# Optimization experiments

Measured on AMD Instinct MI355X. Metric: run time of the kernel, lower is better.

## Reference

```python
import math
import jax, jax.numpy as jnp
import numpy as np

B, S, D, H = 2, 4096, 512, 8
DH = D // H


def setup_inputs() -> dict:
    key = jax.random.key(0)
    ks = jax.random.split(key, 12)
    lim = 1.0 / math.sqrt(D)
    u = lambda k, shp: jax.random.uniform(k, shp, jnp.float32, -lim, lim)
    return {
        "x": jax.random.normal(ks[0], (B, S, D), jnp.float32),
        "gamma": jax.random.uniform(ks[1], (B, S, 1), jnp.float32),
        "Wq": u(ks[2], (D, D)), "bq": u(ks[3], (D,)),
        "Wk": u(ks[4], (D, D)), "bk": u(ks[5], (D,)),
        "Wv": u(ks[6], (D, D)), "bv": u(ks[7], (D,)),
        "Wo": u(ks[8], (D, D)), "bo": u(ks[9], (D,)),
    }


def reference(x, gamma, Wq, bq, Wk, bk, Wv, bv, Wo, bo):
    b, s, d = x.shape
    # projections (torch Linear: x @ W.T + b), split heads -> [B,H,S,DH]
    def proj(W, bias):
        return (x @ W.T + bias).reshape(b, s, H, DH).transpose(0, 2, 1, 3)
    q, k, v = proj(Wq, bq), proj(Wk, bk), proj(Wv, bv)

    scores = jnp.einsum("bhsd,bhtd->bhst", q, k) / math.sqrt(DH)  # [B,H,S,S]
    causal = jnp.triu(jnp.ones((s, s), bool), k=1)  # True above diagonal
    neg_inf = jnp.float32(-jnp.inf)
    scores = jnp.where(causal[None, None], neg_inf, scores)

    # hyperbolic positional bias: -log1p(gamma_i * max(i-j, 0) + 1e-8)
    pos = jnp.arange(s)
    delta = jnp.clip(pos[:, None] - pos[None, :], 0).astype(jnp.float32)  # [S,S]
    gamma_q = gamma[:, :, 0][:, :, None]  # [B,S,1]
    hyper = -jnp.log1p(gamma_q * delta + 1e-8)  # [B,S,S]
    hyper = jnp.where(causal[None], neg_inf, hyper)
    scores = scores + hyper[:, None]  # [B,H,S,S]

    attn = jax.nn.softmax(scores, axis=-1)
    out = jnp.einsum("bhst,bhtd->bhsd", attn, v)  # [B,H,S,DH]
    out = out.transpose(0, 2, 1, 3).reshape(b, s, d)
    return out @ Wo.T + bo
```

## Files before the change

kernel.cpp:

```cpp
#include <hip/hip_runtime.h>
#include <hip/hip_bf16.h>

#define Bb 2
#define Ss 4096
#define Dd 512
#define Hh 8
#define DHh 64

typedef __attribute__((ext_vector_type(8))) short short8;
typedef __attribute__((ext_vector_type(4))) float floatx4;

static __device__ __forceinline__ ushort bfbits(float f) {
  union { __hip_bfloat16 h; ushort u; } cv;
  cv.h = __float2bfloat16(f);
  return cv.u;
}

static __device__ __forceinline__ unsigned int packhi(float a, float b) {
  union { float f; unsigned int u; } ca, cb; ca.f = a; cb.f = b;
  return (ca.u >> 16) | (cb.u & 0xffff0000u);
}

__global__ void cvt_all(const float* __restrict__ x,
                        const float* __restrict__ w0, const float* __restrict__ w1,
                        const float* __restrict__ w2, const float* __restrict__ w3,
                        ushort* __restrict__ out) {
  const int XN4 = (Bb * Ss * Dd) / 4;
  const int WN4 = (Dd * Dd) / 4;
  int i = blockIdx.x * blockDim.x + threadIdx.x;
  if (i >= XN4 + 4 * WN4) return;
  const float* s; int li;
  if (i < XN4) { s = x; li = i; }
  else {
    int t = i - XN4; int j = t >> 16; li = t & (WN4 - 1);
    s = (j == 0) ? w0 : (j == 1) ? w1 : (j == 2) ? w2 : w3;
  }
  float4 f = ((const float4*)s)[li];
  ushort4 u;
  u.x = bfbits(f.x); u.y = bfbits(f.y); u.z = bfbits(f.z); u.w = bfbits(f.w);
  ((ushort4*)out)[i] = u;
}

static __device__ __forceinline__ int vperm(int s0) {
  int kb = (s0 >> 4) & 3, gq = (s0 >> 2) & 3;
  return (s0 & ~63) | ((kb >> 1) << 5) | (gq << 3) | ((kb & 1) << 2);
}

#define LDQK(buf, k0)                                                          \
  _Pragma("unroll")                                                            \
  for (int rb = 0; rb < 4; ++rb)                                               \
    af[buf][rb] = *(const short8*)(ap + (size_t)rb * 16 * 512 + (k0));         \
  _Pragma("unroll")                                                            \
  for (int cb = 0; cb < 4; ++cb)                                               \
    bf[buf][cb] = *(const short8*)(bp + (size_t)cb * 16 * 512 + (k0));

__global__ __launch_bounds__(256) void qkv_gemm(
    const ushort* __restrict__ xb,
    const ushort* __restrict__ Wq, const ushort* __restrict__ Wk, const ushort* __restrict__ Wv,
    const float* __restrict__ bq, const float* __restrict__ bk, const float* __restrict__ bv,
    ushort* __restrict__ qo, ushort* __restrict__ ko, ushort* __restrict__ vo)
{
  int mb = blockIdx.x / 12, rest = blockIdx.x % 12;
  int which = rest >> 2, nb = rest & 3;
  const ushort* Bw  = (which == 0) ? Wq : (which == 1) ? Wk : Wv;
  const float* bias = (which == 0) ? bq : (which == 1) ? bk : bv;
  int lane = threadIdx.x & 63, w = threadIdx.x >> 6;
  int wr = w & 1, wc = w >> 1;
  int g = lane >> 4, ln = lane & 15;
  int m0 = mb * 128 + wr * 64;
  int c0 = nb * 128 + wc * 64;
  const ushort* ap = xb + (size_t)(m0 + ln) * 512 + g * 8;
  const ushort* bp = Bw + (size_t)(c0 + ln) * 512 + g * 8;
  floatx4 acc[4][4] = {};
  short8 af[2][4], bf[2][4];
  LDQK(0, 0)
#pragma unroll
  for (int it = 0; it < 16; ++it) {
    int cur = it & 1;
    if (it < 15) { LDQK(cur ^ 1, (it + 1) * 32) }
#pragma unroll
    for (int rb = 0; rb < 4; ++rb)
#pragma unroll
      for (int cb = 0; cb < 4; ++cb)
        acc[rb][cb] = __builtin_amdgcn_mfma_f32_16x16x32_bf16(af[cur][rb], bf[cur][cb], acc[rb][cb], 0, 0, 0);
  }
  float scale = (which == 0) ? 0.125f : 1.0f;
#pragma unroll
  for (int rb = 0; rb < 4; ++rb)
#pragma unroll
    for (int cb = 0; cb < 4; ++cb) {
      int col = c0 + cb * 16 + ln;
      float bv_ = bias[col];
      int hh = col >> 6, dh = col & 63;
      if (which == 2) {
        int i0 = m0 + rb * 16 + g * 4;
        int bI = i0 >> 12, s0 = i0 & (Ss - 1);
        ushort4 pk;
        pk.x = bfbits(acc[rb][cb][0] + bv_);
        pk.y = bfbits(acc[rb][cb][1] + bv_);
        pk.z = bfbits(acc[rb][cb][2] + bv_);
        pk.w = bfbits(acc[rb][cb][3] + bv_);
        *(ushort4*)(vo + (((size_t)bI * Hh + hh) * DHh + dh) * Ss + vperm(s0)) = pk;
      } else {
        ushort* outp = (which == 0) ? qo : ko;
#pragma unroll
        for (int r = 0; r < 4; ++r) {
          int i = m0 + rb * 16 + g * 4 + r;
          int bI = i >> 12, s = i & (Ss - 1);
          outp[(((size_t)bI * Hh + hh) * Ss + s) * DHh + dh] = bfbits((acc[rb][cb][r] + bv_) * scale);
        }
      }
    }
}

#define LD32(buf, k0)                                                          \
  af[buf][0] = *(const short8*)(ap + (k0));                                    \
  af[buf][1] = *(const short8*)(ap + 16 * 512 + (k0));                         \
  _Pragma("unroll")                                                            \
  for (int ns = 0; ns < 4; ++ns)                                               \
    bfr[buf][ns] = *(const short8*)(bp + (size_t)ns * 16 * 512 + (k0));

__global__ __launch_bounds__(256) void gemm_out(
    const ushort* __restrict__ A, const ushort* __restrict__ Bw,
    const float* __restrict__ bias, float* __restrict__ outp)
{
  int mb = blockIdx.x >> 3, nb = blockIdx.x & 7;
  int lane = threadIdx.x & 63, w = threadIdx.x >> 6;
  int g = lane >> 4, ln = lane & 15;
  int m0 = mb * 128 + w * 32;
  const ushort* ap = A + (size_t)(m0 + ln) * 512 + g * 8;
  const ushort* bp = Bw + (size_t)(nb * 64 + ln) * 512 + g * 8;
  floatx4 acc[2][4] = {};
  short8 af[2][2], bfr[2][4];
  LD32(0, 0)
#pragma unroll
  for (int it = 0; it < 16; ++it) {
    int cur = it & 1;
    if (it < 15) { LD32(cur ^ 1, (it + 1) * 32) }
#pragma unroll
    for (int ns = 0; ns < 4; ++ns) {
      acc[0][ns] = __builtin_amdgcn_mfma_f32_16x16x32_bf16(af[cur][0], bfr[cur][ns], acc[0][ns], 0, 0, 0);
      acc[1][ns] = __builtin_amdgcn_mfma_f32_16x16x32_bf16(af[cur][1], bfr[cur][ns], acc[1][ns], 0, 0, 0);
    }
  }
#pragma unroll
  for (int rb = 0; rb < 2; ++rb)
#pragma unroll
    for (int ns = 0; ns < 4; ++ns) {
      int col = nb * 64 + ns * 16 + ln;
      float bv_ = bias[col];
#pragma unroll
      for (int r = 0; r < 4; ++r)
        outp[(size_t)(m0 + rb * 16 + g * 4 + r) * 512 + col] = acc[rb][ns][r] + bv_;
    }
}

__global__ __launch_bounds__(256, 2) void flash6(
    const ushort* __restrict__ q, const ushort* __restrict__ k,
    const ushort* __restrict__ vt, const float* __restrict__ gamma,
    ushort* __restrict__ o)
{
  __shared__ __align__(16) float Pmrg[2][64][34];
  __shared__ __align__(16) ushort Tb[2][16 * 72];

  int z = blockIdx.x;
  int bh = z & 15, up = z >> 4;
  int b = bh >> 3, hh = bh & 7;
  int tid = threadIdx.x;
  int wv = tid >> 6, lane = tid & 63;
  int qsel = wv >> 1, half = wv & 1;
  int g = lane >> 4, ln = lane & 15;

  const ushort* kp = k + ((size_t)bh * Ss + ln) * DHh + g * 8;
  const ushort* vp = vt + ((size_t)bh * DHh + ln) * Ss + g * 8;

#pragma unroll 1
  for (int rep = 0; rep < 2; ++rep) {
    int u = rep ? (63 - up) : up;
    int t = 2 * u + qsel;
    int q0 = t * 32;
    int ktm = u;
    int nkt = u + 1;
    int h = (nkt + 1 - rep) >> 1;
    int lo = half ? h : 0, hi = half ? nkt : h;

    const ushort* qp = q + ((size_t)bh * Ss + q0 + ln) * DHh + g * 8;
    short8 qf00 = *(const short8*)qp;
    short8 qf01 = *(const short8*)(qp + 32);
    short8 qf10 = *(const short8*)(qp + 16 * DHh);
    short8 qf11 = *(const short8*)(qp + 16 * DHh + 32);

    int qrow0 = q0 + ln, qrow1 = q0 + 16 + ln;
    float gm0 = gamma[(size_t)b * Ss + qrow0];
    float gm1 = gamma[(size_t)b * Ss + qrow1];
    float l2[2] = {0.0f, 0.0f};
    floatx4 oacc[2][4] = {};

    short8 kfl[4], kfh[4], vf[8];
    int kb0 = lo * 64;
#pragma unroll
    for (int ns = 0; ns < 4; ++ns) {
      kfl[ns] = *(const short8*)(kp + (size_t)(kb0 + ns * 16) * DHh);
      kfh[ns] = *(const short8*)(kp + (size_t)(kb0 + ns * 16) * DHh + 32);
    }
#pragma unroll
    for (int cc = 0; cc < 8; ++cc)
      vf[cc] = *(const short8*)(vp + (size_t)((cc & 3) * 16) * Ss + kb0 + (cc >> 2) * 32);

    for (int kt = lo; kt < hi; ++kt) {
      int kbase = kt * 64;
      float sv[2][16];
#pragma unroll
      for (int ns = 0; ns < 4; ++ns) {
        floatx4 z0 = {}, z1 = {};
        z0 = __builtin_amdgcn_mfma_f32_16x16x32_bf16(kfl[ns], qf00, z0, 0, 0, 0);
        z0 = __builtin_amdgcn_mfma_f32_16x16x32_bf16(kfh[ns], qf01, z0, 0, 0, 0);
        z1 = __builtin_amdgcn_mfma_f32_16x16x32_bf16(kfl[ns], qf10, z1, 0, 0, 0);
        z1 = __builtin_amdgcn_mfma_f32_16x16x32_bf16(kfh[ns], qf11, z1, 0, 0, 0);
#pragma unroll
        for (int r = 0; r < 4; ++r) { sv[0][ns * 4 + r] = z0[r]; sv[1][ns * 4 + r] = z1[r]; }
      }
      if (kt + 1 < hi) {
        const ushort* kn = kp + (size_t)(kbase + 64) * DHh;
#pragma unroll
        for (int ns = 0; ns < 4; ++ns) {
          kfl[ns] = *(const short8*)(kn + (size_t)(ns * 16) * DHh);
          kfh[ns] = *(const short8*)(kn + (size_t)(ns * 16) * DHh + 32);
        }
      }
      bool last = (kt == ktm);
      short8 pfrag[2][2];
#pragma unroll
      for (int qb = 0; qb < 2; ++qb) {
        int qrow = qb ? qrow1 : qrow0;
        float gm = qb ? gm1 : gm0;
        int db = qrow - kbase - g * 4;
        if (last) {
#pragma unroll
          for (int e = 0; e < 16; ++e)
            if (db - (e >> 2) * 16 - (e & 3) < 0) sv[qb][e] = -1e30f;
        }
        float fd = (float)db;
        float rs = 0.0f;
#pragma unroll
        for (int e = 0; e < 16; ++e) {
          float delta = fmaxf(fd - (float)((e >> 2) * 16 + (e & 3)), 0.0f);
          float wt = __builtin_amdgcn_rcpf(fmaf(gm, delta, 1.0f));
          float pv = __expf(sv[qb][e]) * wt;
          rs += pv;
          sv[qb][e] = pv;
        }
        l2[qb] += rs;
#pragma unroll
        for (int c = 0; c < 2; ++c) {
          uint4 pkd;
          pkd.x = packhi(sv[qb][8 * c + 0], sv[qb][8 * c + 1]);
          pkd.y = packhi(sv[qb][8 * c + 2], sv[qb][8 * c + 3]);
          pkd.z = packhi(sv[qb][8 * c + 4], sv[qb][8 * c + 5]);
          pkd.w = packhi(sv[qb][8 * c + 6], sv[qb][8 * c + 7]);
          pfrag[qb][c] = *(short8*)&pkd;
        }
      }
#pragma unroll
      for (int c = 0; c < 2; ++c)
#pragma unroll
        for (int ds = 0; ds < 4; ++ds) {
          oacc[0][ds] = __builtin_amdgcn_mfma_f32_16x16x32_bf16(vf[c * 4 + ds], pfrag[0][c], oacc[0][ds], 0, 0, 0);
          oacc[1][ds] = __builtin_amdgcn_mfma_f32_16x16x32_bf16(vf[c * 4 + ds], pfrag[1][c], oacc[1][ds], 0, 0, 0);
        }
      if (kt + 1 < hi) {
#pragma unroll
        for (int cc = 0; cc < 8; ++cc)
          vf[cc] = *(const short8*)(vp + (size_t)((cc & 3) * 16) * Ss + kbase + 64 + (cc >> 2) * 32);
      }
    }

    __syncthreads();
    if (half) {
#pragma unroll
      for (int qb = 0; qb < 2; ++qb)
#pragma unroll
        for (int ds = 0; ds < 4; ++ds)
#pragma unroll
          for (int r = 0; r < 4; ++r)
            Pmrg[qsel][lane][qb * 16 + ds * 4 + r] = oacc[qb][ds][r];
      Pmrg[qsel][lane][32] = l2[0];
      Pmrg[qsel][lane][33] = l2[1];
    }
    __syncthreads();
    if (!half) {
#pragma unroll
      for (int qb = 0; qb < 2; ++qb) {
#pragma unroll
        for (int ds = 0; ds < 4; ++ds)
#pragma unroll
          for (int r = 0; r < 4; ++r)
            oacc[qb][ds][r] += Pmrg[qsel][lane][qb * 16 + ds * 4 + r];
        float l = l2[qb] + Pmrg[qsel][lane][32 + qb];
        l += __shfl_xor(l, 16);
        l += __shfl_xor(l, 32);
        float linv = 1.0f / l;
        ushort* tb = &Tb[qsel][0];
#pragma unroll
        for (int ds = 0; ds < 4; ++ds)
#pragma unroll
          for (int r = 0; r < 4; ++r)
            tb[ln * 72 + ds * 16 + g * 4 + r] = bfbits(oacc[qb][ds][r] * linv);
        short8 v0 = *(const short8*)(tb + ln * 72 + g * 16);
        short8 v1 = *(const short8*)(tb + ln * 72 + g * 16 + 8);
        size_t oa = ((size_t)b * Ss + q0 + qb * 16 + ln) * Dd + hh * DHh + g * 16;
        *(short8*)(o + oa) = v0;
        *(short8*)(o + oa + 8) = v1;
      }
    }
  }
}

extern "C" void kernel_launch(void* const* d_in, const int* in_sizes, int n_in,
                              void* d_out, int out_size, void* d_ws, size_t ws_size,
                              hipStream_t stream) {
  const float* x     = (const float*)d_in[0];
  const float* gamma = (const float*)d_in[1];
  const float* Wq    = (const float*)d_in[2];
  const float* bq    = (const float*)d_in[3];
  const float* Wk    = (const float*)d_in[4];
  const float* bk    = (const float*)d_in[5];
  const float* Wv    = (const float*)d_in[6];
  const float* bv    = (const float*)d_in[7];
  const float* Wo    = (const float*)d_in[8];
  const float* bo    = (const float*)d_in[9];

  const size_t NX = (size_t)Bb * Ss * Dd;
  const size_t NW = (size_t)Dd * Dd;
  ushort* xb  = (ushort*)d_ws;
  ushort* Wqb = xb + NX;
  ushort* Wkb = Wqb + NW;
  ushort* Wvb = Wkb + NW;
  ushort* Wob = Wvb + NW;
  ushort* qb  = Wob + NW;
  ushort* kb  = qb + NX;
  ushort* vtb = kb + NX;
  ushort* ab  = vtb + NX;

  const int total4 = (int)(NX / 4 + 4 * (NW / 4));
  cvt_all<<<(total4 + 255) / 256, 256, 0, stream>>>(x, Wq, Wk, Wv, Wo, xb);

  qkv_gemm<<<64 * 12, 256, 0, stream>>>(xb, Wqb, Wkb, Wvb, bq, bk, bv, qb, kb, vtb);

  flash6<<<512, 256, 0, stream>>>(qb, kb, vtb, gamma, ab);

  gemm_out<<<512, 256, 0, stream>>>(ab, Wob, bo, (float*)d_out);
}
```

Baseline: 282.7 us.

## Split each query tile's key range across four waves and use exp2 softmax

The flash kernel now assigns one 32-row query tile per block and splits its causal key-tile range across all four waves. Partial outputs from three waves are merged through shared memory, and the grid doubles to 1024 blocks with launch bounds raised to 4 blocks per SM. Log2(e) is folded into the Q scale so the kernel can call the hardware exp2 directly, and the fmax clamp on delta is dropped for non-diagonal tiles. The aim is better load balance and occupancy and less SFU/ALU work, at the cost of a larger cross-wave merge and tighter register limits.

```diff
diff --git a/kernel.cpp b/kernel.cpp
--- a/kernel.cpp
+++ b/kernel.cpp
@@ -84,7 +84,7 @@
       for (int cb = 0; cb < 4; ++cb)
         acc[rb][cb] = __builtin_amdgcn_mfma_f32_16x16x32_bf16(af[cur][rb], bf[cur][cb], acc[rb][cb], 0, 0, 0);
   }
-  float scale = (which == 0) ? 0.125f : 1.0f;
+  float scale = (which == 0) ? 0.125f * 1.44269504f : 1.0f;
 #pragma unroll
   for (int rb = 0; rb < 4; ++rb)
 #pragma unroll
@@ -155,20 +155,19 @@
     }
 }
 
-__global__ __launch_bounds__(256, 2) void flash6(
+__global__ __launch_bounds__(256, 4) void flash7(
     const ushort* __restrict__ q, const ushort* __restrict__ k,
     const ushort* __restrict__ vt, const float* __restrict__ gamma,
     ushort* __restrict__ o)
 {
-  __shared__ __align__(16) float Pmrg[2][64][34];
-  __shared__ __align__(16) ushort Tb[2][16 * 72];
+  __shared__ __align__(16) float Pmrg[3][64][34];
+  __shared__ __align__(16) ushort Tb[16 * 72];
 
   int z = blockIdx.x;
-  int bh = z & 15, up = z >> 4;
+  int bh = z & 15, tq = z >> 4;
   int b = bh >> 3, hh = bh & 7;
   int tid = threadIdx.x;
   int wv = tid >> 6, lane = tid & 63;
-  int qsel = wv >> 1, half = wv & 1;
   int g = lane >> 4, ln = lane & 15;
 
   const ushort* kp = k + ((size_t)bh * Ss + ln) * DHh + g * 8;
@@ -176,13 +175,11 @@
 
 #pragma unroll 1
   for (int rep = 0; rep < 2; ++rep) {
-    int u = rep ? (63 - up) : up;
-    int t = 2 * u + qsel;
+    int t = rep ? (127 - tq) : tq;
     int q0 = t * 32;
-    int ktm = u;
-    int nkt = u + 1;
-    int h = (nkt + 1 - rep) >> 1;
-    int lo = half ? h : 0, hi = half ? nkt : h;
+    int nkt = (t >> 1) + 1;
+    int ktm = nkt - 1;
+    int lo = (nkt * wv) >> 2, hi = (nkt * (wv + 1)) >> 2;
 
     const ushort* qp = q + ((size_t)bh * Ss + q0 + ln) * DHh + g * 8;
     short8 qf00 = *(const short8*)qp;
@@ -235,20 +232,29 @@
         int qrow = qb ? qrow1 : qrow0;
         float gm = qb ? gm1 : gm0;
         int db = qrow - kbase - g * 4;
+        float fd = (float)db;
+        float rs = 0.0f;
         if (last) {
 #pragma unroll
           for (int e = 0; e < 16; ++e)
             if (db - (e >> 2) * 16 - (e & 3) < 0) sv[qb][e] = -1e30f;
-        }
-        float fd = (float)db;
-        float rs = 0.0f;
-#pragma unroll
-        for (int e = 0; e < 16; ++e) {
-          float delta = fmaxf(fd - (float)((e >> 2) * 16 + (e & 3)), 0.0f);
-          float wt = __builtin_amdgcn_rcpf(fmaf(gm, delta, 1.0f));
-          float pv = __expf(sv[qb][e]) * wt;
-          rs += pv;
-          sv[qb][e] = pv;
+#pragma unroll
+          for (int e = 0; e < 16; ++e) {
+            float delta = fmaxf(fd - (float)((e >> 2) * 16 + (e & 3)), 0.0f);
+            float wt = __builtin_amdgcn_rcpf(fmaf(gm, delta, 1.0f));
+            float pv = __builtin_amdgcn_exp2f(sv[qb][e]) * wt;
+            rs += pv;
+            sv[qb][e] = pv;
+          }
+        } else {
+#pragma unroll
+          for (int e = 0; e < 16; ++e) {
+            float delta = fd - (float)((e >> 2) * 16 + (e & 3));
+            float wt = __builtin_amdgcn_rcpf(fmaf(gm, delta, 1.0f));
+            float pv = __builtin_amdgcn_exp2f(sv[qb][e]) * wt;
+            rs += pv;
+            sv[qb][e] = pv;
+          }
         }
         l2[qb] += rs;
 #pragma unroll
@@ -276,38 +282,41 @@
     }
 
     __syncthreads();
-    if (half) {
+    if (wv) {
 #pragma unroll
       for (int qb = 0; qb < 2; ++qb)
 #pragma unroll
         for (int ds = 0; ds < 4; ++ds)
 #pragma unroll
           for (int r = 0; r < 4; ++r)
-            Pmrg[qsel][lane][qb * 16 + ds * 4 + r] = oacc[qb][ds][r];
-      Pmrg[qsel][lane][32] = l2[0];
-      Pmrg[qsel][lane][33] = l2[1];
+            Pmrg[wv - 1][lane][qb * 16 + ds * 4 + r] = oacc[qb][ds][r];
+      Pmrg[wv - 1][lane][32] = l2[0];
+      Pmrg[wv - 1][lane][33] = l2[1];
     }
     __syncthreads();
-    if (!half) {
+    if (!wv) {
 #pragma unroll
       for (int qb = 0; qb < 2; ++qb) {
-#pragma unroll
-        for (int ds = 0; ds < 4; ++ds)
-#pragma unroll
-          for (int r = 0; r < 4; ++r)
-            oacc[qb][ds][r] += Pmrg[qsel][lane][qb * 16 + ds * 4 + r];
-        float l = l2[qb] + Pmrg[qsel][lane][32 + qb];
+        float l = l2[qb];
+#pragma unroll
+        for (int w2 = 0; w2 < 3; ++w2) {
+#pragma unroll
+          for (int ds = 0; ds < 4; ++ds)
+#pragma unroll
+            for (int r = 0; r < 4; ++r)
+              oacc[qb][ds][r] += Pmrg[w2][lane][qb * 16 + ds * 4 + r];
+          l += Pmrg[w2][lane][32 + qb];
+        }
         l += __shfl_xor(l, 16);
         l += __shfl_xor(l, 32);
         float linv = 1.0f / l;
-        ushort* tb = &Tb[qsel][0];
 #pragma unroll
         for (int ds = 0; ds < 4; ++ds)
 #pragma unroll
           for (int r = 0; r < 4; ++r)
-            tb[ln * 72 + ds * 16 + g * 4 + r] = bfbits(oacc[qb][ds][r] * linv);
-        short8 v0 = *(const short8*)(tb + ln * 72 + g * 16);
-        short8 v1 = *(const short8*)(tb + ln * 72 + g * 16 + 8);
+            Tb[ln * 72 + ds * 16 + g * 4 + r] = bfbits(oacc[qb][ds][r] * linv);
+        short8 v0 = *(const short8*)(Tb + ln * 72 + g * 16);
+        short8 v1 = *(const short8*)(Tb + ln * 72 + g * 16 + 8);
         size_t oa = ((size_t)b * Ss + q0 + qb * 16 + ln) * Dd + hh * DHh + g * 16;
         *(short8*)(o + oa) = v0;
         *(short8*)(o + oa + 8) = v1;
@@ -347,7 +356,7 @@
 
   qkv_gemm<<<64 * 12, 256, 0, stream>>>(xb, Wqb, Wkb, Wvb, bq, bk, bv, qb, kb, vtb);
 
-  flash6<<<512, 256, 0, stream>>>(qb, kb, vtb, gamma, ab);
+  flash7<<<1024, 256, 0, stream>>>(qb, kb, vtb, gamma, ab);
 
   gemm_out<<<512, 256, 0, stream>>>(ab, Wob, bo, (float*)d_out);
 }
```

After: 599.9 us. +112.2%, slower.
